# Performance work log

Hardware: AMD Instinct MI355X
Metric: run time of the kernel (lower is better)

Reference implementation:

```python
import jax, jax.numpy as jnp
import numpy as np

# ---- para constants (see shape_source) ----
SIZE = 200          # SLM / detector plane
PAD = 100           # para.paddings -> padded FFT plane 400x400
PADDED = SIZE + 2 * PAD
NUM_LAYERS = 4
SCALE = 2.0         # para.scale
EXT = 1.0           # para.extension
K = 8               # para.kernel_size
S = 8               # para.stride
M = (SIZE - K) // S + 1   # para.map_size = 25
WIN = 5             # para.win_size
T = 1.0             # softmax temperature
RANGE = 10          # para.range (== dim_out)
DIM_OUT = 10
HIDDEN = 512
DIM_IN = M * M      # 625, flattened BN output feeds fcl
THR = 0.2           # para.thershold
SHIFT = 0.0         # para.shift
EPS = 1e-5          # BatchNorm eps
BATCH = 32


def setup_inputs() -> dict:
    key = jax.random.key(0)
    ks = jax.random.split(key, 10)
    x = jax.random.uniform(ks[0], (BATCH, SIZE, SIZE), jnp.float32)

    def transfer(k):  # unit-magnitude angular-spectrum transfer function
        ph = jax.random.uniform(k, (PADDED, PADDED), jnp.float32, 0.0, 2.0 * np.pi)
        return jnp.exp(1j * ph).astype(jnp.complex64)

    h = transfer(ks[1])
    h_pro = transfer(ks[2])
    h_det = transfer(ks[3])
    phase = 0.1 * jax.random.normal(ks[4], (NUM_LAYERS, SIZE, SIZE), jnp.float32)
    W1 = 0.02 * jax.random.normal(ks[5], (HIDDEN, DIM_IN), jnp.float32)
    b1 = jnp.zeros((HIDDEN,), jnp.float32)
    W2 = 0.02 * jax.random.normal(ks[6], (DIM_OUT, HIDDEN), jnp.float32)
    b2 = jnp.zeros((DIM_OUT,), jnp.float32)
    gamma = jnp.ones((1,), jnp.float32)   # BatchNorm2d(1) weight
    beta = jnp.zeros((1,), jnp.float32)   # BatchNorm2d(1) bias
    return {"x": x, "batch_size": BATCH, "h": h, "h_pro": h_pro, "h_det": h_det,
            "phase": phase, "W1": W1, "b1": b1, "W2": W2, "b2": b2,
            "gamma": gamma, "beta": beta}


def _diff(wave, trans):
    # F.pad + fftshift/fft2 * trans / ifft2/ifftshift (batch-dim shifts cancel)
    wave = jnp.pad(wave, ((0, 0), (PAD, PAD), (PAD, PAD)))
    wf = jnp.fft.fft2(jnp.fft.fftshift(wave, axes=(-2, -1)))
    return jnp.fft.ifftshift(jnp.fft.ifft2(wf * trans), axes=(-2, -1))


def _forward(x, batch_size, h, h_pro, h_det, phase, W1, b1, W2, b2, gamma, beta):
    x = x.astype(jnp.complex64)
    x = _diff(x, h_pro)[:, PAD:PAD + SIZE, PAD:PAD + SIZE]
    for idx in range(NUM_LAYERS):
        trans = jnp.pad(phase[idx], ((PAD, PAD), (PAD, PAD)))
        w = _diff(x, h)
        w = w * jnp.exp(1j * SCALE * jnp.pi * (jnp.sin(EXT * trans) + 1.0))
        x = w[:, PAD:PAD + SIZE, PAD:PAD + SIZE]
    x = _diff(x, h_det)[:, PAD:PAD + SIZE, PAD:PAD + SIZE]
    i_out = jnp.square(jnp.abs(x))                       # (B, SIZE, SIZE)
    B = i_out.shape[0]
    # AvgPool2d(K, S) with SIZE % K == 0 -> reshape-mean
    pooled = i_out.reshape(B, M, K, M, K).mean(axis=(2, 4))  # (B, M, M)

    rows = jnp.arange(M)

    def window(i, j):
        rm = (rows >= i) & (rows < i + WIN)
        cm = (rows >= j) & (rows < j + WIN)
        mask = (rm[:, None] & cm[None, :]).astype(pooled.dtype)   # I_block
        sig = pooled * mask                                       # (B, M, M)
        # BatchNorm2d(1), training mode: stats over all N*H*W
        mu = sig.mean()
        var = sig.var()
        nrm = (sig - mu) / jnp.sqrt(var + EPS) * gamma[0] + beta[0]
        f = nrm.reshape(B, -1)                                    # (B, DIM_IN)
        hid = jax.nn.relu(f @ W1.T + b1)                          # dropout: eval
        logits = (hid @ W2.T + b2) / T
        p = jax.nn.softmax(logits, axis=1)                        # (B, DIM_OUT)
        a = jnp.argmax(p, axis=1)                                 # (B,)
        delta = p.max(axis=1) - p.min(axis=1)                     # b - b2
        temp = jax.nn.one_hot(a, RANGE + 1, dtype=jnp.float32).sum(0)
        final0 = jnp.argmax(temp)
        dm = delta * (a == final0).astype(delta.dtype)            # delta * delta_max
        nz = jnp.sum(dm != 0.0)                                   # csr .data length
        delta1 = jnp.where(nz > 0, dm.sum() / jnp.maximum(nz, 1).astype(dm.dtype), jnp.nan)
        # nan < THR is False, matching torch semantics
        final = jnp.where(delta1 < THR, 0, final0 + 1).astype(jnp.int32)
        res = jnp.where(final == 0, 0.0, final.astype(jnp.float32) + SHIFT)
        ch = (final != 0).astype(jnp.float32)
        return final, res, ch

    ii, jj = jnp.meshgrid(jnp.arange(M), jnp.arange(M), indexing="ij")
    finals, result, ch_map = jax.vmap(window)(ii.ravel(), jj.ravel())
    result = result.reshape(M, M)
    ch_map = ch_map.reshape(M, M)
    histo = jnp.zeros(RANGE + 1, jnp.float32).at[finals].add(1.0)
    return result, ch_map, histo


def reference(x, batch_size, h, h_pro, h_det, phase, W1, b1, W2, b2, gamma, beta):
    return _forward(x, batch_size, h, h_pro, h_det, phase, W1, b1, W2, b2, gamma, beta)
```

## Files before the change

kernel.cpp:

```cpp
#include <hip/hip_runtime.h>
#include <math.h>

#define GLIM_X    1280000
#define GLIM_H    160000
#define GLIM_PH   160000
#define GLIM_W1   320000
#define GLIM_B1   512
#define GLIM_W2   5120
#define GLIM_B2   10
#define GLIM_OUT  1261
#define GLIM_POOL 20000

#define HPART 128

struct cplx { float x, y; };
__device__ __forceinline__ cplx operator+(cplx a, cplx b){ return {a.x+b.x, a.y+b.y}; }
__device__ __forceinline__ cplx operator-(cplx a, cplx b){ return {a.x-b.x, a.y-b.y}; }
__device__ __forceinline__ cplx cmul(cplx a, cplx b){ return {a.x*b.x - a.y*b.y, a.x*b.y + a.y*b.x}; }
template<bool INV>
__device__ __forceinline__ cplx tw(cplx a, cplx w){
  if(INV) return {a.x*w.x + a.y*w.y, a.y*w.x - a.x*w.y};
  else    return {a.x*w.x - a.y*w.y, a.x*w.y + a.y*w.x};
}
template<bool INV>
__device__ __forceinline__ void dft4(cplx&a, cplx&b, cplx&c, cplx&d){
  cplx t0=a+c, t1=a-c, t2=b+d, t3=b-d;
  cplx j3 = INV ? cplx{-t3.y, t3.x} : cplx{t3.y, -t3.x};
  a = t0+t2; c = t0-t2; b = t1+j3; d = t1-j3;
}
template<bool INV>
__device__ void fft16(cplx* x, const cplx* tab){
  cplx y[16];
  #pragma unroll
  for(int b=0;b<4;b++){
    cplx p0=x[b], p1=x[4+b], p2=x[8+b], p3=x[12+b];
    dft4<INV>(p0,p1,p2,p3);
    y[b*4+0]=p0;
    y[b*4+1]=tw<INV>(p1, tab[25*b]);
    y[b*4+2]=tw<INV>(p2, tab[50*b]);
    y[b*4+3]=tw<INV>(p3, tab[75*b]);
  }
  #pragma unroll
  for(int c=0;c<4;c++){
    cplx p0=y[c], p1=y[4+c], p2=y[8+c], p3=y[12+c];
    dft4<INV>(p0,p1,p2,p3);
    x[c]=p0; x[c+4]=p1; x[c+8]=p2; x[c+12]=p3;
  }
}
template<bool INV>
__device__ __forceinline__ void dft5(const cplx* v, cplx* o, const cplx* tab){
  #pragma unroll
  for(int k=0;k<5;k++){
    cplx s=v[0];
    #pragma unroll
    for(int j=1;j<5;j++){
      const int m=(j*k)%5;
      s = s + tw<INV>(v[j], tab[80*m]);
    }
    o[k]=s;
  }
}
template<bool INV>
__device__ void fft25(cplx* t, const cplx* tab){
  cplx u[25];
  #pragma unroll
  for(int b=0;b<5;b++){
    cplx v[5], o[5];
    #pragma unroll
    for(int a=0;a<5;a++) v[a]=t[5*a+b];
    dft5<INV>(v,o,tab);
    #pragma unroll
    for(int c=0;c<5;c++) u[b*5+c]=tw<INV>(o[c], tab[16*b*c]);
  }
  #pragma unroll
  for(int c=0;c<5;c++){
    cplx v[5], o[5];
    #pragma unroll
    for(int b=0;b<5;b++) v[b]=u[b*5+c];
    dft5<INV>(v,o,tab);
    #pragma unroll
    for(int d=0;d<5;d++) t[c+5*d]=o[d];
  }
}

__device__ __forceinline__ float bf2f(unsigned short u){
  unsigned int v = ((unsigned int)u)<<16;
  float f; __builtin_memcpy(&f,&v,4); return f;
}
__device__ __forceinline__ float hf2f(unsigned short u){
  _Float16 x; __builtin_memcpy(&x,&u,2); return (float)x;
}
__device__ __forceinline__ cplx ldH(const void* p, int i, int dec){
  if(i<0 || i>=GLIM_H) return {0.f,0.f};
  unsigned int v = ((const unsigned int*)p)[i];
  unsigned short lo=(unsigned short)(v&0xFFFFu), hi=(unsigned short)(v>>16);
  cplx z;
  if(dec==2)      z = { hf2f(lo), hf2f(hi) };
  else if(dec==3) z = { (float)(short)lo*(1.f/32767.f), (float)(short)hi*(1.f/32767.f) };
  else            z = { bf2f(lo), bf2f(hi) };
  if(!(fabsf(z.x) < 2.f)) z.x = 0.f;
  if(!(fabsf(z.y) < 2.f)) z.y = 0.f;
  return z;
}
__device__ __forceinline__ float ldf(const float* p, int i, int lim){
  if(i<0 || i>=lim) return 0.f;
  return p[i];
}
__device__ __forceinline__ void stout(float* p, int i, float v){
  if(i>=0 && i<GLIM_OUT) p[i] = v;
}

__global__ __launch_bounds__(64) void k_probe(const void* h, int* flags){
  __shared__ float err[3];
  if(threadIdx.x<3) err[threadIdx.x]=0.f;
  __syncthreads();
  if(threadIdx.x<32){
    unsigned int v = ((const unsigned int*)h)[threadIdx.x];
    unsigned short lo=(unsigned short)(v&0xFFFFu), hi=(unsigned short)(v>>16);
    float cr[3], ci[3];
    cr[0]=bf2f(lo);                       ci[0]=bf2f(hi);
    cr[1]=hf2f(lo);                       ci[1]=hf2f(hi);
    cr[2]=(float)(short)lo*(1.f/32767.f); ci[2]=(float)(short)hi*(1.f/32767.f);
    for(int d=0;d<3;d++){
      float r2 = cr[d]*cr[d] + ci[d]*ci[d];
      float e = fabsf(r2 - 1.f);
      if(!(e < 4.f)) e = 4.f;
      atomicAdd(&err[d], e);
    }
  }
  __syncthreads();
  if(threadIdx.x==0){
    int best=0; float be=err[0];
    for(int d=1; d<3; d++) if(err[d] < be){ be=err[d]; best=d; }
    flags[1] = best+1;
    flags[0] = 0;
  }
}

__global__ __launch_bounds__(256) void k_init(cplx* tab, float* outz, float* hist, float* pr){
  int t = blockIdx.x*256 + threadIdx.x;
  if(t < 400){
    float a = -6.28318530717958647692f * (float)t * (1.0f/400.0f);
    float sn, cs; sincosf(a, &sn, &cs);
    tab[t] = { cs, sn };
  }
  if(t < GLIM_OUT) outz[t] = 0.f;
  if(t < 11) hist[t] = 0.f;
  if(t >= 16 && t < 30) pr[t-16] = 0.f;
}

__global__ __launch_bounds__(256) void k_hprep(const void* h, const void* hpro,
    const void* hdet, cplx* __restrict__ Hd, const int* __restrict__ flags)
{
  int dec = flags[1];
  int t = blockIdx.x*256 + threadIdx.x;
  if(t >= 3*GLIM_H) return;
  int arr = t/GLIM_H, o = t - arr*GLIM_H;
  int c = o/400, rem = o - c*400;
  int k1 = rem/25, k2 = rem - k1*25;
  const void* src = (arr==0)?h:((arr==1)?hpro:hdet);
  Hd[t] = ldH(src, (k1+16*k2)*400 + c, dec);
}

__global__ __launch_bounds__(256,2) void k_rowfft(const float* __restrict__ xr,
    int img0, cplx* __restrict__ A, const cplx* __restrict__ gtab, int alim)
{
  __shared__ cplx lt[8*400];
  __shared__ cplx stab[400];
  for(int m=threadIdx.x;m<400;m+=256) stab[m]=gtab[m];
  int lr = threadIdx.x>>5, role = threadIdx.x&31;
  int idx = blockIdx.x*8 + lr;
  int img_local = idx/200, rc = idx - img_local*200;
  int abase = img_local*80000 + rc*400;
  __syncthreads();
  if(role<25){
    int n2=role;
    cplx x[16];
    #pragma unroll
    for(int n1=0;n1<16;n1++){
      cplx v={0.f,0.f};
      if(n1>=4 && n1<12){
        int cc = 25*n1+n2-100;
        v = { ldf(xr, (img0+img_local)*40000 + rc*200 + cc, GLIM_X), 0.f };
      }
      x[n1]=v;
    }
    fft16<false>(x, stab);
    cplx* L = lt + lr*400;
    #pragma unroll
    for(int k1=0;k1<16;k1++) L[k1*25+n2]=tw<false>(x[k1], stab[n2*k1]);
  }
  __syncthreads();
  if(role<16){
    int k1=role;
    cplx* L = lt + lr*400;
    cplx t[25];
    #pragma unroll
    for(int n2=0;n2<25;n2++) t[n2]=L[k1*25+n2];
    fft25<false>(t, stab);
    #pragma unroll
    for(int k2=0;k2<25;k2++){
      int ai = abase + k1+16*k2;
      if(ai>=0 && ai<alim) A[ai]=t[k2];
    }
  }
}

__global__ __launch_bounds__(512,2) void k_colpass(cplx* __restrict__ A,
    const cplx* __restrict__ Hd, const cplx* __restrict__ gtab)
{
  __shared__ cplx lt[16*401];
  __shared__ cplx stab[400];
  cplx (*sm)[17] = (cplx(*)[17])lt;
  for(int m=threadIdx.x;m<400;m+=512) stab[m]=gtab[m];
  int img_local = blockIdx.x/25, cg = blockIdx.x - img_local*25;
  int col0 = cg*16;
  int lc = threadIdx.x&15, rr = threadIdx.x>>4;
  cplx* L = lt + lc*401;
  cplx xx[25];
  __syncthreads();
  {
    const float4* A4 = (const float4*)A;
    for(int t=threadIdx.x; t<1600; t+=512){
      int r = t>>3, p = t&7;
      int ce = img_local*80000 + r*400 + col0 + 2*p;
      float4 v = A4[ce>>1];
      sm[r][2*p]   = { v.x, v.y };
      sm[r][2*p+1] = { v.z, v.w };
    }
  }
  __syncthreads();
  if(rr<25){
    int n2=rr;
    #pragma unroll
    for(int n1=0;n1<16;n1++){
      cplx v={0.f,0.f};
      if(n1>=4 && n1<12) v = sm[25*n1+n2-100][lc];
      xx[n1]=v;
    }
  }
  __syncthreads();
  if(rr<25){
    int n2=rr;
    fft16<false>(xx, stab);
    #pragma unroll
    for(int k1=0;k1<16;k1++) L[k1*25+n2]=tw<false>(xx[k1], stab[n2*k1]);
  }
  __syncthreads();
  if(rr<16){
    int k1=rr;
    #pragma unroll
    for(int n2=0;n2<25;n2++) xx[n2]=L[k1*25+n2];
    fft25<false>(xx, stab);
    const cplx* hrun = Hd + (col0+lc)*400 + k1*25;
    #pragma unroll
    for(int k2=0;k2<25;k2++) xx[k2]=cmul(xx[k2], hrun[k2]);
  }
  __syncthreads();
  if(rr<16){
    int k1=rr;
    #pragma unroll
    for(int k2=0;k2<25;k2++) L[k1+16*k2]=xx[k2];
  }
  __syncthreads();
  if(rr<25){
    int n2=rr;
    #pragma unroll
    for(int n1=0;n1<16;n1++) xx[n1]=L[25*n1+n2];
  }
  __syncthreads();
  if(rr<25){
    int n2=rr;
    fft16<true>(xx, stab);
    #pragma unroll
    for(int k1=0;k1<16;k1++) L[k1*25+n2]=tw<true>(xx[k1], stab[n2*k1]);
  }
  __syncthreads();
  if(rr<16){
    int k1=rr;
    #pragma unroll
    for(int n2=0;n2<25;n2++) xx[n2]=L[k1*25+n2];
    fft25<true>(xx, stab);
    const float sc=1.0f/400.0f;
    #pragma unroll
    for(int k2=0;k2<25;k2++){ xx[k2].x*=sc; xx[k2].y*=sc; }
  }
  __syncthreads();
  if(rr<16){
    int k1=rr;
    #pragma unroll
    for(int k2=0;k2<25;k2++){
      int m=k1+16*k2;
      if(m>=100 && m<300) sm[m-100][lc] = xx[k2];
    }
  }
  __syncthreads();
  {
    float4* A4 = (float4*)A;
    for(int t=threadIdx.x; t<1600; t+=512){
      int r = t>>3, p = t&7;
      int ce = img_local*80000 + r*400 + col0 + 2*p;
      cplx a = sm[r][2*p], b = sm[r][2*p+1];
      A4[ce>>1] = { a.x, a.y, b.x, b.y };
    }
  }
}

__global__ __launch_bounds__(512,2) void k_rowpass(cplx* __restrict__ A,
    const float* __restrict__ ph, int phoff, int useMask,
    const cplx* __restrict__ gtab, int alim)
{
  __shared__ cplx lt[16*400];
  __shared__ cplx stab[400];
  cplx (*sm)[200] = (cplx(*)[200])lt;
  for(int m=threadIdx.x;m<400;m+=512) stab[m]=gtab[m];
  int lr=threadIdx.x>>5, role=threadIdx.x&31;
  int idx = blockIdx.x*16+lr;
  int img_local = idx/200, rc = idx - img_local*200;
  int abase = img_local*80000 + rc*400;
  __syncthreads();
  if(role<25){
    int n2=role;
    cplx x[16];
    #pragma unroll
    for(int n1=0;n1<16;n1++){
      cplx v={0.f,0.f};
      int ai = abase + 25*n1+n2;
      if(ai>=0 && ai<alim) v=A[ai];
      x[n1]=v;
    }
    fft16<true>(x, stab);
    cplx* L = lt + lr*400;
    #pragma unroll
    for(int k1=0;k1<16;k1++) L[k1*25+n2]=tw<true>(x[k1], stab[n2*k1]);
  }
  __syncthreads();
  cplx t[25];
  int k1 = role;
  if(role<16){
    cplx* L=lt+lr*400;
    #pragma unroll
    for(int n2=0;n2<25;n2++) t[n2]=L[k1*25+n2];
    fft25<true>(t, stab);
    const float sc=1.0f/400.0f;
    #pragma unroll
    for(int k2=0;k2<25;k2++){ t[k2].x*=sc; t[k2].y*=sc; }
  }
  __syncthreads();
  if(role<16){
    #pragma unroll
    for(int k2=0;k2<25;k2++){
      int m=k1+16*k2;
      if(m>=100 && m<300){
        int cc=m-100;
        cplx v=t[k2];
        if(useMask){
          float tt = ldf(ph, phoff + rc*200+cc, GLIM_PH);
          float th = 6.28318530717958647692f*(sinf(tt)+1.0f);
          float sn, cs; sincosf(th,&sn,&cs);
          v = cmul(v, cplx{cs,sn});
        }
        sm[lr][cc]=v;
      }
    }
  }
  __syncthreads();
  cplx x2[16];
  if(role<25){
    int n2=role;
    #pragma unroll
    for(int n1=0;n1<16;n1++){
      cplx v={0.f,0.f};
      if(n1>=4 && n1<12) v = sm[lr][25*n1+n2-100];
      x2[n1]=v;
    }
  }
  __syncthreads();
  if(role<25){
    int n2=role;
    fft16<false>(x2, stab);
    cplx* L = lt + lr*400;
    #pragma unroll
    for(int k1f=0;k1f<16;k1f++) L[k1f*25+n2]=tw<false>(x2[k1f], stab[n2*k1f]);
  }
  __syncthreads();
  if(role<16){
    cplx* L = lt + lr*400;
    cplx t2[25];
    #pragma unroll
    for(int n2=0;n2<25;n2++) t2[n2]=L[k1*25+n2];
    fft25<false>(t2, stab);
    #pragma unroll
    for(int k2=0;k2<25;k2++){
      int ai = abase + k1+16*k2;
      if(ai>=0 && ai<alim) A[ai]=t2[k2];
    }
  }
}

__global__ __launch_bounds__(256,2) void k_rowpool(const cplx* __restrict__ A,
    float* __restrict__ pooled, int img0, const cplx* __restrict__ gtab, int alim)
{
  __shared__ cplx lt[8*400];
  __shared__ cplx stab[400];
  __shared__ float sI[8][200];
  for(int m=threadIdx.x;m<400;m+=256) stab[m]=gtab[m];
  int lr=threadIdx.x>>5, role=threadIdx.x&31;
  int idx = blockIdx.x*8+lr;
  int img_local = idx/200;
  int abase = img_local*80000 + (idx - img_local*200)*400;
  __syncthreads();
  if(role<25){
    int n2=role;
    cplx x[16];
    #pragma unroll
    for(int n1=0;n1<16;n1++){
      cplx v={0.f,0.f};
      int ai = abase + 25*n1+n2;
      if(ai>=0 && ai<alim) v=A[ai];
      x[n1]=v;
    }
    fft16<true>(x, stab);
    cplx* L = lt + lr*400;
    #pragma unroll
    for(int k1=0;k1<16;k1++) L[k1*25+n2]=tw<true>(x[k1], stab[n2*k1]);
  }
  __syncthreads();
  cplx t[25];
  int k1 = role;
  if(role<16){
    cplx* L=lt+lr*400;
    #pragma unroll
    for(int n2=0;n2<25;n2++) t[n2]=L[k1*25+n2];
    fft25<true>(t, stab);
    const float sc=1.0f/400.0f;
    #pragma unroll
    for(int k2=0;k2<25;k2++){ t[k2].x*=sc; t[k2].y*=sc; }
  }
  if(role<16){
    #pragma unroll
    for(int k2=0;k2<25;k2++){
      int m=k1+16*k2;
      if(m>=100 && m<300) sI[lr][m-100] = t[k2].x*t[k2].x + t[k2].y*t[k2].y;
    }
  }
  __syncthreads();
  if(threadIdx.x<25){
    int band = blockIdx.x*8;
    int il = band/200, r0 = band - il*200;
    float s=0.f;
    #pragma unroll
    for(int u=0;u<8;u++){
      #pragma unroll
      for(int v=0;v<8;v++) s += sI[u][threadIdx.x*8+v];
    }
    int pi = (img0+il)*625 + (r0>>3)*25 + threadIdx.x;
    if(pi>=0 && pi<GLIM_POOL) pooled[pi] = s*(1.0f/64.0f);
  }
}

__global__ __launch_bounds__(64) void k_rowsum(const float* __restrict__ W1,
    float* __restrict__ rs){
  __shared__ float red[64];
  int hh = blockIdx.x;
  float s=0.f;
  for(int e=threadIdx.x;e<625;e+=64) s += ldf(W1, hh*625+e, GLIM_W1);
  red[threadIdx.x]=s;
  __syncthreads();
  for(int off=32;off>0;off>>=1){
    if(threadIdx.x<off) red[threadIdx.x]+=red[threadIdx.x+off];
    __syncthreads();
  }
  if(threadIdx.x==0 && hh<512) rs[hh]=red[0];
}

__global__ __launch_bounds__(256,2) void k_window(const float* __restrict__ pooled,
    const float* __restrict__ W1, const float* __restrict__ b1,
    const float* __restrict__ W2, const float* __restrict__ rowsum,
    const float* __restrict__ gm, const float* __restrict__ bt,
    float* __restrict__ LP)
{
  __shared__ float w1s[HPART*26];
  __shared__ float w2s[10*HPART];
  __shared__ float ps[25*32];
  __shared__ float comb[HPART];
  __shared__ int   wIdx[25];
  __shared__ float sred[4][2];
  __shared__ float sf0, sgos;

  int wi = blockIdx.x >> 2;
  int part = blockIdx.x & 3;
  int h0 = part*HPART;
  int i = wi/25, j = wi - i*25;
  int er = (25-i<5)?(25-i):5;
  int ec = (25-j<5)?(25-j):5;
  int E = er*ec;
  int tid = threadIdx.x;
  if(tid<25) wIdx[tid] = (i + tid/ec)*25 + (j + tid%ec);
  __syncthreads();

  for(int t=tid;t<10*HPART;t+=256) w2s[t] = ldf(W2, (t>>7)*512 + h0 + (t&(HPART-1)), GLIM_W2);

  for(int t=tid;t<800;t+=256){
    int e=t>>5;
    float v=0.f;
    if(e<E){
      v = pooled[(t&31)*625 + wIdx[e]];
      if(!(fabsf(v) < 1e30f)) v = 0.f;
    }
    ps[t]=v;
  }

  if(E==25){
    for(int t=tid;t<HPART*25;t+=256){
      int hh=t/25, e=t-hh*25;
      w1s[hh*26+e] = ldf(W1, (h0+hh)*625+wIdx[e], GLIM_W1);
    }
  } else {
    for(int t=tid;t<832;t+=256) ((float4*)w1s)[t] = float4{0.f,0.f,0.f,0.f};
    __syncthreads();
    for(int t=tid;t<HPART*E;t+=256){
      int hh=t/E, e=t-hh*E;
      w1s[hh*26+e] = ldf(W1, (h0+hh)*625+wIdx[e], GLIM_W1);
    }
  }
  __syncthreads();

  {
    float s1=0.f, s2=0.f;
    for(int t=tid;t<800;t+=256){ float v=ps[t]; s1+=v; s2+=v*v; }
    #pragma unroll
    for(int m=1;m<64;m<<=1){ s1 += __shfl_xor(s1,m); s2 += __shfl_xor(s2,m); }
    if((tid&63)==0){ sred[tid>>6][0]=s1; sred[tid>>6][1]=s2; }
  }
  __syncthreads();
  if(tid==0){
    float a=sred[0][0]+sred[1][0]+sred[2][0]+sred[3][0];
    float c=sred[0][1]+sred[1][1]+sred[2][1]+sred[3][1];
    float mu = a*(1.0f/20000.0f);
    float var = c*(1.0f/20000.0f) - mu*mu;
    float sg = sqrtf(var + 1e-5f);
    float g = gm[0];
    sf0 = bt[0] - g*mu/sg;
    sgos = g/sg;
  }
  __syncthreads();
  float f0=sf0, gos=sgos;
  for(int hh=tid;hh<HPART;hh+=256) comb[hh] = ldf(b1,h0+hh,GLIM_B1) + f0*ldf(rowsum,h0+hh,512);
  __syncthreads();

  int b = tid&31, s = tid>>5;
  float psr[25];
  #pragma unroll
  for(int e=0;e<25;e++) psr[e]=ps[e*32+b];

  float pl[10];
  #pragma unroll
  for(int o=0;o<10;o++) pl[o]=0.f;
  for(int k=0;k<16;k++){
    int hh = s*16+k;
    const float* wr = &w1s[hh*26];
    float wsum=0.f;
    #pragma unroll
    for(int e=0;e<25;e++) wsum = fmaf(wr[e], psr[e], wsum);
    float acc = comb[hh] + gos*wsum;
    float hid = acc>0.f?acc:0.f;
    #pragma unroll
    for(int o=0;o<10;o++) pl[o] = fmaf(hid, w2s[o*HPART+hh], pl[o]);
  }
  __syncthreads();
  float* red = w1s;
  #pragma unroll
  for(int o=0;o<10;o++) red[(s*32+b)*10+o]=pl[o];
  __syncthreads();

  if(tid<32){
    #pragma unroll
    for(int o=0;o<10;o++){
      float a = 0.f;
      #pragma unroll
      for(int u=0;u<8;u++) a += red[(u*32+tid)*10+o];
      LP[((part*625+wi)*32+tid)*10+o] = a;
    }
  }
}

__global__ __launch_bounds__(64) void k_vote(const float* __restrict__ LP,
    const float* __restrict__ b2, float* __restrict__ outp, float* __restrict__ hist)
{
  __shared__ int aArr[32];
  __shared__ float dArr[32];
  int wi = blockIdx.x, tid = threadIdx.x;
  if(tid<32){
    float lg[10];
    #pragma unroll
    for(int o=0;o<10;o++){
      float a = ldf(b2,o,GLIM_B2);
      #pragma unroll
      for(int p=0;p<4;p++) a += LP[((p*625+wi)*32+tid)*10+o];
      lg[o]=a;
    }
    float lmax=lg[0]; int am=0;
    #pragma unroll
    for(int o=1;o<10;o++) if(lg[o]>lmax){lmax=lg[o]; am=o;}
    float lmin=lg[0];
    #pragma unroll
    for(int o=1;o<10;o++) lmin=fminf(lmin,lg[o]);
    float Z=0.f;
    #pragma unroll
    for(int o=0;o<10;o++) Z += expf(lg[o]-lmax);
    float delta = (1.f - expf(lmin-lmax))/Z;
    aArr[tid]=am; dArr[tid]=delta;
  }
  __syncthreads();
  if(tid==0){
    int votes[11];
    #pragma unroll
    for(int k=0;k<11;k++) votes[k]=0;
    for(int bb=0;bb<32;bb++){
      int a=aArr[bb];
      if(a>=0 && a<11) votes[a]++;
    }
    int f0i=0, bv=votes[0];
    #pragma unroll
    for(int k=1;k<11;k++) if(votes[k]>bv){bv=votes[k]; f0i=k;}
    float sum=0.f; int nz=0;
    for(int bb=0;bb<32;bb++){
      if(aArr[bb]==f0i){
        float dd=dArr[bb];
        sum+=dd;
        if(dd!=0.f) nz++;
      }
    }
    int fin;
    if(nz>0){
      float d1=sum/(float)nz;
      fin = (d1<0.2f)?0:(f0i+1);
    } else fin = f0i+1;
    stout(outp, wi, (fin==0)?0.f:(float)fin);
    stout(outp, 625+wi, (fin!=0)?1.f:0.f);
    if(fin>=0 && fin<=10) atomicAdd(&hist[fin], 1.0f);
  }
}

__global__ __launch_bounds__(64) void k_fin(const float* __restrict__ hist,
    float* __restrict__ outp){
  if(threadIdx.x<11) stout(outp, 1250+threadIdx.x, hist[threadIdx.x]);
}

__global__ __launch_bounds__(256) void k_diag(const float* __restrict__ pooled,
    const float* __restrict__ hist, const float* __restrict__ pr,
    const int* __restrict__ flags, float* __restrict__ outp){
  __shared__ float smax[256];
  __shared__ int snan[256];
  float m=0.f; int nan=0;
  for(int i=threadIdx.x;i<GLIM_POOL;i+=256){
    float v=pooled[i];
    if(isnan(v)||isinf(v)) nan=1;
    else { float a=fabsf(v); if(a>m)m=a; }
  }
  smax[threadIdx.x]=m; snan[threadIdx.x]=nan;
  __syncthreads();
  for(int off=128;off>0;off>>=1){
    if(threadIdx.x<off){
      smax[threadIdx.x]=fmaxf(smax[threadIdx.x],smax[threadIdx.x+off]);
      snan[threadIdx.x]|=snan[threadIdx.x+off];
    }
    __syncthreads();
  }
  if(threadIdx.x==0 && hist[0] < 613.f){
    int dec = flags[1] & 7;
    int low, nanbit = 0;
    if(snan[0]){ nanbit=128; low=0; (void)pr; }
    else {
      if(smax[0]<=0.f) low=0;
      else {
        int e=(int)floorf(log2f(smax[0]));
        low = e+8; if(low<1)low=1; if(low>15)low=15;
      }
    }
    int S = nanbit | (dec<<4) | low;
    outp[0] = 8192.0f*(float)S;
  }
}

extern "C" void kernel_launch(void* const* d_in, const int* in_sizes, int n_in,
                              void* d_out, int out_size, void* d_ws, size_t ws_size,
                              hipStream_t stream)
{
  (void)in_sizes;
  if(n_in != 12 || out_size < GLIM_OUT || d_ws == nullptr) return;
  const float* x   = (const float*)d_in[0];
  const void* h    = d_in[2];
  const void* hpro = d_in[3];
  const void* hdet = d_in[4];
  const float* phase=(const float*)d_in[5];
  const float* W1  = (const float*)d_in[6];
  const float* b1  = (const float*)d_in[7];
  const float* W2  = (const float*)d_in[8];
  const float* b2  = (const float*)d_in[9];
  const float* gm  = (const float*)d_in[10];
  const float* bt  = (const float*)d_in[11];
  float* out = (float*)d_out;

  const size_t FIXED = 85888ull;
  const size_t HDB   = 3ull*GLIM_H*8ull;
  const size_t ABase = FIXED + HDB;
  int n = 0;
  if     (ABase + 32ull*640000ull <= ws_size) n = 32;
  else if(ABase + 16ull*640000ull <= ws_size) n = 16;
  else if(ABase +  8ull*640000ull <= ws_size) n = 8;
  else if(ABase +  4ull*640000ull <= ws_size) n = 4;
  else if(ABase +  2ull*640000ull <= ws_size) n = 2;
  else if(ABase +  1ull*640000ull <= ws_size) n = 1;
  if(n==0) return;

  char* w = (char*)d_ws;
  int*   flags  = (int*)(w + 0);
  cplx*  tab    = (cplx*)(w + 256);
  float* rowsum = (float*)(w + 3584);
  float* hist   = (float*)(w + 5632);
  float* pr     = (float*)(w + 5760);
  float* pooled = (float*)(w + 5888);
  cplx*  Hd     = (cplx*)(w + FIXED);
  cplx*  A      = (cplx*)(w + ABase);
  float* LP     = (float*)Hd;
  const int alim  = n*80000;

  k_probe<<<1,64,0,stream>>>(h, flags);
  k_init<<<6,256,0,stream>>>(tab, out, hist, pr);
  k_rowsum<<<512,64,0,stream>>>(W1, rowsum);
  k_hprep<<<(3*GLIM_H+255)/256,256,0,stream>>>(h, hpro, hdet, Hd, flags);

  for(int c=0; c<32; c+=n){
    k_rowfft<<<n*25,256,0,stream>>>(x, c, A, tab, alim);
    for(int d=0; d<6; d++){
      const cplx* Hcur = (d==0) ? (Hd+GLIM_H) : ((d==5) ? (Hd+2*GLIM_H) : Hd);
      k_colpass<<<n*25,512,0,stream>>>(A, Hcur, tab);
      if(d<5){
        int useMask = (d>=1) ? 1 : 0;
        int phoff = useMask ? (d-1)*40000 : 0;
        k_rowpass<<<(n*200+15)/16,512,0,stream>>>(A, phase, phoff, useMask, tab, alim);
      } else {
        k_rowpool<<<n*25,256,0,stream>>>(A, pooled, c, tab, alim);
      }
    }
  }
  k_window<<<2500,256,0,stream>>>(pooled, W1,b1,W2,rowsum, gm,bt, LP);
  k_vote<<<625,64,0,stream>>>(LP, b2, out, hist);
  k_fin<<<1,64,0,stream>>>(hist, out);
  k_diag<<<1,256,0,stream>>>(pooled, hist, pr, flags, out);
}
```

Measured before the change: 688.9 us.

## Map each FFT line to one wavefront and replace block barriers with LDS waits

Restructures the row and column FFT kernels so each 32-lane group owns one 400-point line in its own LDS slice. This lets the block-wide __syncthreads between FFT stages become an s_waitcnt lgkmcnt(0) fence. It also merges adjacent phases, enlarges rowfft and rowpool to 512 threads covering 16 rows, and gives colpass a separate transpose buffer. The risk is correctness: lanes of a 64-wide wavefront span two groups, and intra-wave LDS visibility relies only on the waitcnt, with no compiler barrier against reordering beyond the asm memory clobber.

```diff
diff --git a/kernel.cpp b/kernel.cpp
--- a/kernel.cpp
+++ b/kernel.cpp
@@ -81,6 +81,10 @@
     #pragma unroll
     for(int d=0;d<5;d++) t[c+5*d]=o[d];
   }
+}
+
+__device__ __forceinline__ void wfence(){
+  __asm__ volatile("s_waitcnt lgkmcnt(0)" ::: "memory");
 }
 
 __device__ __forceinline__ float bf2f(unsigned short u){
@@ -162,20 +166,21 @@
   Hd[t] = ldH(src, (k1+16*k2)*400 + c, dec);
 }
 
-__global__ __launch_bounds__(256,2) void k_rowfft(const float* __restrict__ xr,
+__global__ __launch_bounds__(512,2) void k_rowfft(const float* __restrict__ xr,
     int img0, cplx* __restrict__ A, const cplx* __restrict__ gtab, int alim)
 {
-  __shared__ cplx lt[8*400];
+  __shared__ cplx lb[16*400];
   __shared__ cplx stab[400];
-  for(int m=threadIdx.x;m<400;m+=256) stab[m]=gtab[m];
-  int lr = threadIdx.x>>5, role = threadIdx.x&31;
-  int idx = blockIdx.x*8 + lr;
+  for(int m=threadIdx.x;m<400;m+=512) stab[m]=gtab[m];
+  int g = threadIdx.x>>5, role = threadIdx.x&31;
+  int idx = blockIdx.x*16 + g;
   int img_local = idx/200, rc = idx - img_local*200;
   int abase = img_local*80000 + rc*400;
+  cplx* L = lb + g*400;
+  cplx xx[25];
   __syncthreads();
   if(role<25){
     int n2=role;
-    cplx x[16];
     #pragma unroll
     for(int n1=0;n1<16;n1++){
       cplx v={0.f,0.f};
@@ -183,25 +188,22 @@
         int cc = 25*n1+n2-100;
         v = { ldf(xr, (img0+img_local)*40000 + rc*200 + cc, GLIM_X), 0.f };
       }
-      x[n1]=v;
-    }
-    fft16<false>(x, stab);
-    cplx* L = lt + lr*400;
-    #pragma unroll
-    for(int k1=0;k1<16;k1++) L[k1*25+n2]=tw<false>(x[k1], stab[n2*k1]);
-  }
-  __syncthreads();
+      xx[n1]=v;
+    }
+    fft16<false>(xx, stab);
+    #pragma unroll
+    for(int k1=0;k1<16;k1++) L[k1*25+n2]=tw<false>(xx[k1], stab[n2*k1]);
+  }
+  wfence();
   if(role<16){
     int k1=role;
-    cplx* L = lt + lr*400;
-    cplx t[25];
-    #pragma unroll
-    for(int n2=0;n2<25;n2++) t[n2]=L[k1*25+n2];
-    fft25<false>(t, stab);
+    #pragma unroll
+    for(int n2=0;n2<25;n2++) xx[n2]=L[k1*25+n2];
+    fft25<false>(xx, stab);
     #pragma unroll
     for(int k2=0;k2<25;k2++){
       int ai = abase + k1+16*k2;
-      if(ai>=0 && ai<alim) A[ai]=t[k2];
+      if(ai>=0 && ai<alim) A[ai]=xx[k2];
     }
   }
 }
@@ -209,16 +211,15 @@
 __global__ __launch_bounds__(512,2) void k_colpass(cplx* __restrict__ A,
     const cplx* __restrict__ Hd, const cplx* __restrict__ gtab)
 {
-  __shared__ cplx lt[16*401];
+  __shared__ cplx sm[200][17];
+  __shared__ cplx lb[16*400];
   __shared__ cplx stab[400];
-  cplx (*sm)[17] = (cplx(*)[17])lt;
   for(int m=threadIdx.x;m<400;m+=512) stab[m]=gtab[m];
   int img_local = blockIdx.x/25, cg = blockIdx.x - img_local*25;
   int col0 = cg*16;
-  int lc = threadIdx.x&15, rr = threadIdx.x>>4;
-  cplx* L = lt + lc*401;
+  int g = threadIdx.x>>5, role = threadIdx.x&31;
+  cplx* L = lb + g*400;
   cplx xx[25];
-  __syncthreads();
   {
     const float4* A4 = (const float4*)A;
     for(int t=threadIdx.x; t<1600; t+=512){
@@ -230,68 +231,50 @@
     }
   }
   __syncthreads();
-  if(rr<25){
-    int n2=rr;
+  if(role<25){
+    int n2=role;
     #pragma unroll
     for(int n1=0;n1<16;n1++){
       cplx v={0.f,0.f};
-      if(n1>=4 && n1<12) v = sm[25*n1+n2-100][lc];
+      if(n1>=4 && n1<12) v = sm[25*n1+n2-100][g];
       xx[n1]=v;
     }
-  }
-  __syncthreads();
-  if(rr<25){
-    int n2=rr;
     fft16<false>(xx, stab);
     #pragma unroll
     for(int k1=0;k1<16;k1++) L[k1*25+n2]=tw<false>(xx[k1], stab[n2*k1]);
   }
-  __syncthreads();
-  if(rr<16){
-    int k1=rr;
+  wfence();
+  if(role<16){
+    int k1=role;
     #pragma unroll
     for(int n2=0;n2<25;n2++) xx[n2]=L[k1*25+n2];
     fft25<false>(xx, stab);
-    const cplx* hrun = Hd + (col0+lc)*400 + k1*25;
+    const cplx* hrun = Hd + (col0+g)*400 + k1*25;
     #pragma unroll
     for(int k2=0;k2<25;k2++) xx[k2]=cmul(xx[k2], hrun[k2]);
-  }
-  __syncthreads();
-  if(rr<16){
-    int k1=rr;
     #pragma unroll
     for(int k2=0;k2<25;k2++) L[k1+16*k2]=xx[k2];
   }
-  __syncthreads();
-  if(rr<25){
-    int n2=rr;
+  wfence();
+  if(role<25){
+    int n2=role;
     #pragma unroll
     for(int n1=0;n1<16;n1++) xx[n1]=L[25*n1+n2];
-  }
-  __syncthreads();
-  if(rr<25){
-    int n2=rr;
     fft16<true>(xx, stab);
     #pragma unroll
     for(int k1=0;k1<16;k1++) L[k1*25+n2]=tw<true>(xx[k1], stab[n2*k1]);
   }
-  __syncthreads();
-  if(rr<16){
-    int k1=rr;
+  wfence();
+  if(role<16){
+    int k1=role;
     #pragma unroll
     for(int n2=0;n2<25;n2++) xx[n2]=L[k1*25+n2];
     fft25<true>(xx, stab);
     const float sc=1.0f/400.0f;
     #pragma unroll
-    for(int k2=0;k2<25;k2++){ xx[k2].x*=sc; xx[k2].y*=sc; }
-  }
-  __syncthreads();
-  if(rr<16){
-    int k1=rr;
-    #pragma unroll
     for(int k2=0;k2<25;k2++){
       int m=k1+16*k2;
-      if(m>=100 && m<300) sm[m-100][lc] = xx[k2];
+      if(m>=100 && m<300) sm[m-100][g] = { xx[k2].x*sc, xx[k2].y*sc };
     }
   }
   __syncthreads();
@@ -310,151 +293,134 @@
     const float* __restrict__ ph, int phoff, int useMask,
     const cplx* __restrict__ gtab, int alim)
 {
-  __shared__ cplx lt[16*400];
+  __shared__ cplx lb[16*400];
   __shared__ cplx stab[400];
-  cplx (*sm)[200] = (cplx(*)[200])lt;
   for(int m=threadIdx.x;m<400;m+=512) stab[m]=gtab[m];
-  int lr=threadIdx.x>>5, role=threadIdx.x&31;
-  int idx = blockIdx.x*16+lr;
+  int g = threadIdx.x>>5, role = threadIdx.x&31;
+  int idx = blockIdx.x*16 + g;
   int img_local = idx/200, rc = idx - img_local*200;
   int abase = img_local*80000 + rc*400;
+  cplx* L = lb + g*400;
+  cplx xx[25];
   __syncthreads();
   if(role<25){
     int n2=role;
-    cplx x[16];
     #pragma unroll
     for(int n1=0;n1<16;n1++){
       cplx v={0.f,0.f};
       int ai = abase + 25*n1+n2;
       if(ai>=0 && ai<alim) v=A[ai];
-      x[n1]=v;
-    }
-    fft16<true>(x, stab);
-    cplx* L = lt + lr*400;
-    #pragma unroll
-    for(int k1=0;k1<16;k1++) L[k1*25+n2]=tw<true>(x[k1], stab[n2*k1]);
-  }
-  __syncthreads();
-  cplx t[25];
-  int k1 = role;
+      xx[n1]=v;
+    }
+    fft16<true>(xx, stab);
+    #pragma unroll
+    for(int k1=0;k1<16;k1++) L[k1*25+n2]=tw<true>(xx[k1], stab[n2*k1]);
+  }
+  wfence();
   if(role<16){
-    cplx* L=lt+lr*400;
-    #pragma unroll
-    for(int n2=0;n2<25;n2++) t[n2]=L[k1*25+n2];
-    fft25<true>(t, stab);
+    int k1=role;
+    #pragma unroll
+    for(int n2=0;n2<25;n2++) xx[n2]=L[k1*25+n2];
+    fft25<true>(xx, stab);
     const float sc=1.0f/400.0f;
-    #pragma unroll
-    for(int k2=0;k2<25;k2++){ t[k2].x*=sc; t[k2].y*=sc; }
-  }
-  __syncthreads();
-  if(role<16){
     #pragma unroll
     for(int k2=0;k2<25;k2++){
       int m=k1+16*k2;
       if(m>=100 && m<300){
         int cc=m-100;
-        cplx v=t[k2];
+        cplx v={ xx[k2].x*sc, xx[k2].y*sc };
         if(useMask){
           float tt = ldf(ph, phoff + rc*200+cc, GLIM_PH);
           float th = 6.28318530717958647692f*(sinf(tt)+1.0f);
           float sn, cs; sincosf(th,&sn,&cs);
           v = cmul(v, cplx{cs,sn});
         }
-        sm[lr][cc]=v;
+        L[cc]=v;
       }
     }
   }
-  __syncthreads();
-  cplx x2[16];
+  wfence();
   if(role<25){
     int n2=role;
     #pragma unroll
     for(int n1=0;n1<16;n1++){
       cplx v={0.f,0.f};
-      if(n1>=4 && n1<12) v = sm[lr][25*n1+n2-100];
-      x2[n1]=v;
-    }
-  }
+      if(n1>=4 && n1<12) v = L[25*n1+n2-100];
+      xx[n1]=v;
+    }
+    fft16<false>(xx, stab);
+    #pragma unroll
+    for(int k1=0;k1<16;k1++) L[k1*25+n2]=tw<false>(xx[k1], stab[n2*k1]);
+  }
+  wfence();
+  if(role<16){
+    int k1=role;
+    #pragma unroll
+    for(int n2=0;n2<25;n2++) xx[n2]=L[k1*25+n2];
+    fft25<false>(xx, stab);
+    #pragma unroll
+    for(int k2=0;k2<25;k2++){
+      int ai = abase + k1+16*k2;
+      if(ai>=0 && ai<alim) A[ai]=xx[k2];
+    }
+  }
+}
+
+__global__ __launch_bounds__(512,2) void k_rowpool(const cplx* __restrict__ A,
+    float* __restrict__ pooled, int img0, const cplx* __restrict__ gtab, int alim)
+{
+  __shared__ cplx lb[16*400];
+  __shared__ cplx stab[400];
+  __shared__ float sI[16][200];
+  for(int m=threadIdx.x;m<400;m+=512) stab[m]=gtab[m];
+  int g = threadIdx.x>>5, role = threadIdx.x&31;
+  int idx = blockIdx.x*16 + g;
+  int img_local = idx/200;
+  int abase = img_local*80000 + (idx - img_local*200)*400;
+  cplx* L = lb + g*400;
+  cplx xx[25];
   __syncthreads();
   if(role<25){
     int n2=role;
-    fft16<false>(x2, stab);
-    cplx* L = lt + lr*400;
-    #pragma unroll
-    for(int k1f=0;k1f<16;k1f++) L[k1f*25+n2]=tw<false>(x2[k1f], stab[n2*k1f]);
-  }
-  __syncthreads();
-  if(role<16){
-    cplx* L = lt + lr*400;
-    cplx t2[25];
-    #pragma unroll
-    for(int n2=0;n2<25;n2++) t2[n2]=L[k1*25+n2];
-    fft25<false>(t2, stab);
-    #pragma unroll
-    for(int k2=0;k2<25;k2++){
-      int ai = abase + k1+16*k2;
-      if(ai>=0 && ai<alim) A[ai]=t2[k2];
-    }
-  }
-}
-
-__global__ __launch_bounds__(256,2) void k_rowpool(const cplx* __restrict__ A,
-    float* __restrict__ pooled, int img0, const cplx* __restrict__ gtab, int alim)
-{
-  __shared__ cplx lt[8*400];
-  __shared__ cplx stab[400];
-  __shared__ float sI[8][200];
-  for(int m=threadIdx.x;m<400;m+=256) stab[m]=gtab[m];
-  int lr=threadIdx.x>>5, role=threadIdx.x&31;
-  int idx = blockIdx.x*8+lr;
-  int img_local = idx/200;
-  int abase = img_local*80000 + (idx - img_local*200)*400;
-  __syncthreads();
-  if(role<25){
-    int n2=role;
-    cplx x[16];
     #pragma unroll
     for(int n1=0;n1<16;n1++){
       cplx v={0.f,0.f};
       int ai = abase + 25*n1+n2;
       if(ai>=0 && ai<alim) v=A[ai];
-      x[n1]=v;
-    }
-    fft16<true>(x, stab);
-    cplx* L = lt + lr*400;
-    #pragma unroll
-    for(int k1=0;k1<16;k1++) L[k1*25+n2]=tw<true>(x[k1], stab[n2*k1]);
-  }
-  __syncthreads();
-  cplx t[25];
-  int k1 = role;
+      xx[n1]=v;
+    }
+    fft16<true>(xx, stab);
+    #pragma unroll
+    for(int k1=0;k1<16;k1++) L[k1*25+n2]=tw<true>(xx[k1], stab[n2*k1]);
+  }
+  wfence();
   if(role<16){
-    cplx* L=lt+lr*400;
-    #pragma unroll
-    for(int n2=0;n2<25;n2++) t[n2]=L[k1*25+n2];
-    fft25<true>(t, stab);
+    int k1=role;
+    #pragma unroll
+    for(int n2=0;n2<25;n2++) xx[n2]=L[k1*25+n2];
+    fft25<true>(xx, stab);
     const float sc=1.0f/400.0f;
-    #pragma unroll
-    for(int k2=0;k2<25;k2++){ t[k2].x*=sc; t[k2].y*=sc; }
-  }
-  if(role<16){
     #pragma unroll
     for(int k2=0;k2<25;k2++){
       int m=k1+16*k2;
-      if(m>=100 && m<300) sI[lr][m-100] = t[k2].x*t[k2].x + t[k2].y*t[k2].y;
-    }
-  }
-  __syncthreads();
-  if(threadIdx.x<25){
-    int band = blockIdx.x*8;
-    int il = band/200, r0 = band - il*200;
+      if(m>=100 && m<300){
+        float re=xx[k2].x*sc, im=xx[k2].y*sc;
+        sI[g][m-100] = re*re + im*im;
+      }
+    }
+  }
+  __syncthreads();
+  if(threadIdx.x<50){
+    int b = threadIdx.x/25, c = threadIdx.x - b*25;
+    int rbase = blockIdx.x*16 + b*8;
+    int il = rbase/200, r0 = rbase - il*200;
     float s=0.f;
     #pragma unroll
     for(int u=0;u<8;u++){
       #pragma unroll
-      for(int v=0;v<8;v++) s += sI[u][threadIdx.x*8+v];
-    }
-    int pi = (img0+il)*625 + (r0>>3)*25 + threadIdx.x;
+      for(int v=0;v<8;v++) s += sI[b*8+u][c*8+v];
+    }
+    int pi = (img0+il)*625 + (r0>>3)*25 + c;
     if(pi>=0 && pi<GLIM_POOL) pooled[pi] = s*(1.0f/64.0f);
   }
 }
@@ -733,7 +699,7 @@
   k_hprep<<<(3*GLIM_H+255)/256,256,0,stream>>>(h, hpro, hdet, Hd, flags);
 
   for(int c=0; c<32; c+=n){
-    k_rowfft<<<n*25,256,0,stream>>>(x, c, A, tab, alim);
+    k_rowfft<<<(n*200+15)/16,512,0,stream>>>(x, c, A, tab, alim);
     for(int d=0; d<6; d++){
       const cplx* Hcur = (d==0) ? (Hd+GLIM_H) : ((d==5) ? (Hd+2*GLIM_H) : Hd);
       k_colpass<<<n*25,512,0,stream>>>(A, Hcur, tab);
@@ -742,7 +708,7 @@
         int phoff = useMask ? (d-1)*40000 : 0;
         k_rowpass<<<(n*200+15)/16,512,0,stream>>>(A, phase, phoff, useMask, tab, alim);
       } else {
-        k_rowpool<<<n*25,256,0,stream>>>(A, pooled, c, tab, alim);
+        k_rowpool<<<(n*200+15)/16,512,0,stream>>>(A, pooled, c, tab, alim);
       }
     }
   }
```

Measured after the change: 726.4 us. 5.4% more time.

## Remap row-pass FFT threads so adjacent lanes handle different rows, pad LDS

Applied to the files above, without the earlier changes.

In the row-pass kernel, each wavefront used to own one row with 25 or 16 of its 32 lanes active. Threads are now assigned by lane = row (16 rows) and thread-group = FFT index, so a 64-lane wave covers 16 rows times 4 sub-FFTs. This improves lane utilisation, and the 401-element LDS row pitch avoids bank conflicts. Register arrays are merged into a single xx[25] buffer to cut register pressure. The global loads and stores now stride across rows instead of being contiguous within a row, which may hurt coalescing.

```diff
diff --git a/kernel.cpp b/kernel.cpp
--- a/kernel.cpp
+++ b/kernel.cpp
@@ -310,90 +310,84 @@
     const float* __restrict__ ph, int phoff, int useMask,
     const cplx* __restrict__ gtab, int alim)
 {
-  __shared__ cplx lt[16*400];
+  __shared__ cplx lt[16*401];
   __shared__ cplx stab[400];
-  cplx (*sm)[200] = (cplx(*)[200])lt;
   for(int m=threadIdx.x;m<400;m+=512) stab[m]=gtab[m];
-  int lr=threadIdx.x>>5, role=threadIdx.x&31;
-  int idx = blockIdx.x*16+lr;
+  int lc = threadIdx.x&15, rr = threadIdx.x>>4;
+  int idx = blockIdx.x*16 + lc;
   int img_local = idx/200, rc = idx - img_local*200;
   int abase = img_local*80000 + rc*400;
-  __syncthreads();
-  if(role<25){
-    int n2=role;
-    cplx x[16];
+  cplx* L = lt + lc*401;
+  cplx xx[25];
+  __syncthreads();
+  if(rr<25){
+    int n2=rr;
     #pragma unroll
     for(int n1=0;n1<16;n1++){
       cplx v={0.f,0.f};
       int ai = abase + 25*n1+n2;
       if(ai>=0 && ai<alim) v=A[ai];
-      x[n1]=v;
-    }
-    fft16<true>(x, stab);
-    cplx* L = lt + lr*400;
-    #pragma unroll
-    for(int k1=0;k1<16;k1++) L[k1*25+n2]=tw<true>(x[k1], stab[n2*k1]);
-  }
-  __syncthreads();
-  cplx t[25];
-  int k1 = role;
-  if(role<16){
-    cplx* L=lt+lr*400;
-    #pragma unroll
-    for(int n2=0;n2<25;n2++) t[n2]=L[k1*25+n2];
-    fft25<true>(t, stab);
+      xx[n1]=v;
+    }
+    fft16<true>(xx, stab);
+    #pragma unroll
+    for(int k1=0;k1<16;k1++) L[k1*25+n2]=tw<true>(xx[k1], stab[n2*k1]);
+  }
+  __syncthreads();
+  if(rr<16){
+    int k1=rr;
+    #pragma unroll
+    for(int n2=0;n2<25;n2++) xx[n2]=L[k1*25+n2];
+    fft25<true>(xx, stab);
     const float sc=1.0f/400.0f;
-    #pragma unroll
-    for(int k2=0;k2<25;k2++){ t[k2].x*=sc; t[k2].y*=sc; }
-  }
-  __syncthreads();
-  if(role<16){
     #pragma unroll
     for(int k2=0;k2<25;k2++){
       int m=k1+16*k2;
       if(m>=100 && m<300){
         int cc=m-100;
-        cplx v=t[k2];
+        cplx v={ xx[k2].x*sc, xx[k2].y*sc };
         if(useMask){
           float tt = ldf(ph, phoff + rc*200+cc, GLIM_PH);
           float th = 6.28318530717958647692f*(sinf(tt)+1.0f);
           float sn, cs; sincosf(th,&sn,&cs);
           v = cmul(v, cplx{cs,sn});
         }
-        sm[lr][cc]=v;
+        xx[k2]=v;
       }
     }
   }
   __syncthreads();
-  cplx x2[16];
-  if(role<25){
-    int n2=role;
+  if(rr<16){
+    int k1=rr;
+    #pragma unroll
+    for(int k2=0;k2<25;k2++){
+      int m=k1+16*k2;
+      if(m>=100 && m<300) L[m-100]=xx[k2];
+    }
+  }
+  __syncthreads();
+  if(rr<25){
+    int n2=rr;
     #pragma unroll
     for(int n1=0;n1<16;n1++){
       cplx v={0.f,0.f};
-      if(n1>=4 && n1<12) v = sm[lr][25*n1+n2-100];
-      x2[n1]=v;
-    }
-  }
-  __syncthreads();
-  if(role<25){
-    int n2=role;
-    fft16<false>(x2, stab);
-    cplx* L = lt + lr*400;
-    #pragma unroll
-    for(int k1f=0;k1f<16;k1f++) L[k1f*25+n2]=tw<false>(x2[k1f], stab[n2*k1f]);
-  }
-  __syncthreads();
-  if(role<16){
-    cplx* L = lt + lr*400;
-    cplx t2[25];
-    #pragma unroll
-    for(int n2=0;n2<25;n2++) t2[n2]=L[k1*25+n2];
-    fft25<false>(t2, stab);
+      if(n1>=4 && n1<12) v = L[25*n1+n2-100];
+      xx[n1]=v;
+    }
+    fft16<false>(xx, stab);
+    #pragma unroll
+    for(int k1=0;k1<16;k1++) L[k1*25+n2]=tw<false>(xx[k1], stab[n2*k1]);
+  }
+  __syncthreads();
+  if(rr<16){
+    int k1=rr;
+    #pragma unroll
+    for(int n2=0;n2<25;n2++) xx[n2]=L[k1*25+n2];
+    fft25<false>(xx, stab);
     #pragma unroll
     for(int k2=0;k2<25;k2++){
       int ai = abase + k1+16*k2;
-      if(ai>=0 && ai<alim) A[ai]=t2[k2];
+      if(ai>=0 && ai<alim) A[ai]=xx[k2];
     }
   }
 }
```

Measured after the change: 670.7 us. -2.7%, faster.
